# Optimization experiments

Hardware: AMD Instinct MI355X
Metric: run time of the kernel (lower is better)

The kernel has to match this reference:

```python
import jax, jax.numpy as jnp
import numpy as np

H, DH, C, K = 8, 128, 200, 15  # heads, head_dim, context_size, conv kernel
SCALE = DH ** -0.5
EPS = 1e-5


def layernorm(x, g, b):
    mu = jnp.mean(x, axis=-1, keepdims=True)
    var = jnp.mean(jnp.square(x - mu), axis=-1, keepdims=True)
    return (x - mu) * jax.lax.rsqrt(var + EPS) * g + b


def feedforward(x, ln_g, ln_b, up_w, up_b, down_w, down_b):
    h = layernorm(x, ln_g, ln_b)
    h = jax.nn.silu(h @ up_w + up_b)
    return h @ down_w + down_b


def attention(x, dist, ln_g, ln_b, wq, wkv, wo, wo_b, rel_emb):
    h = layernorm(x, ln_g, ln_b)
    b, f, d = h.shape
    nb = f // C  # num_features chosen divisible by context_size (no remainder path)
    q = (h @ wq).reshape(b, nb, C, H, DH).transpose(0, 1, 3, 2, 4)   # [b,nb,H,C,dh]
    kv = h @ wkv
    k, v = jnp.split(kv, 2, axis=-1)
    k = k.reshape(b, nb, C, H, DH).transpose(0, 1, 3, 2, 4)
    v = v.reshape(b, nb, C, H, DH).transpose(0, 1, 3, 2, 4)
    rel = rel_emb[dist]                                              # [C,C,dh]
    pos_attn = jnp.einsum('bnhid,ijd->bnhij', q, rel) * SCALE
    scores = jnp.einsum('bnhid,bnhjd->bnhij', q, k) * SCALE + pos_attn
    probs = jax.nn.softmax(scores, axis=-1)
    out = jnp.einsum('bnhij,bnhjd->bnhid', probs, v)
    out = out.transpose(0, 1, 3, 2, 4).reshape(b, f, H * DH)
    return out @ wo + wo_b


def conv_module(x, ln_g, ln_b, up_w, up_b, dw_w, bn_g, bn_b, bn_mean, bn_var, down_w, down_b):
    h = layernorm(x, ln_g, ln_b)
    h = h @ up_w + up_b                         # pointwise conv == linear; [b,L,2*inner]
    a, gate = jnp.split(h, 2, axis=-1)
    h = a * jax.nn.sigmoid(gate)                # GLU over channel dim
    h = h.transpose(0, 2, 1)                    # [b,inner,L]
    pad = K // 2
    h = jax.lax.conv_general_dilated(
        h, dw_w[:, None, :], window_strides=(1,), padding=[(pad, pad)],
        dimension_numbers=('NCH', 'OIH', 'NCH'), feature_group_count=h.shape[1])
    # BatchNorm1d in eval mode (running stats)
    h = (h - bn_mean[None, :, None]) * jax.lax.rsqrt(bn_var[None, :, None] + EPS)
    h = h * bn_g[None, :, None] + bn_b[None, :, None]
    h = jax.nn.silu(h)
    h = h.transpose(0, 2, 1) @ down_w + down_b  # [b,L,hidden]
    return h


def block_forward(x, attention_dists,
                  ff1_ln_g, ff1_ln_b, ff1_up_w, ff1_up_b, ff1_down_w, ff1_down_b,
                  attn_ln_g, attn_ln_b, wq, wkv, wo, wo_b, rel_emb,
                  conv_ln_g, conv_ln_b, conv_up_w, conv_up_b, dw_w,
                  bn_g, bn_b, bn_mean, bn_var, conv_down_w, conv_down_b,
                  ff2_ln_g, ff2_ln_b, ff2_up_w, ff2_up_b, ff2_down_w, ff2_down_b,
                  post_ln_g, post_ln_b):
    x = 0.5 * feedforward(x, ff1_ln_g, ff1_ln_b, ff1_up_w, ff1_up_b, ff1_down_w, ff1_down_b) + x
    x = attention(x, attention_dists, attn_ln_g, attn_ln_b, wq, wkv, wo, wo_b, rel_emb) + x
    x = conv_module(x, conv_ln_g, conv_ln_b, conv_up_w, conv_up_b, dw_w,
                    bn_g, bn_b, bn_mean, bn_var, conv_down_w, conv_down_b) + x
    x = 0.5 * feedforward(x, ff2_ln_g, ff2_ln_b, ff2_up_w, ff2_up_b, ff2_down_w, ff2_down_b) + x
    return layernorm(x, post_ln_g, post_ln_b)


def setup_inputs() -> dict:
    key = jax.random.key(0)
    ks = iter(jax.random.split(key, 40))
    d, dff, inner = 1024, 4096, 2048
    r = lambda shape, s=0.02: (jax.random.normal(next(ks), shape, jnp.float32) * s)
    inp = {
        'x': jax.random.normal(next(ks), (8, 2000, d), jnp.float32),
        'attention_dists': jax.random.randint(next(ks), (C, C), 0, 1025, jnp.int32),
        'ff1_ln_g': jnp.ones((d,)), 'ff1_ln_b': jnp.zeros((d,)),
        'ff1_up_w': r((d, dff)), 'ff1_up_b': jnp.zeros((dff,)),
        'ff1_down_w': r((dff, d)), 'ff1_down_b': jnp.zeros((d,)),
        'attn_ln_g': jnp.ones((d,)), 'attn_ln_b': jnp.zeros((d,)),
        'wq': r((d, H * DH)), 'wkv': r((d, 2 * H * DH)),
        'wo': r((H * DH, d)), 'wo_b': jnp.zeros((d,)),
        'rel_emb': r((2 * 512 + 1, DH)),
        'conv_ln_g': jnp.ones((d,)), 'conv_ln_b': jnp.zeros((d,)),
        'conv_up_w': r((d, 2 * inner)), 'conv_up_b': jnp.zeros((2 * inner,)),
        'dw_w': r((inner, K)),
        'bn_g': jnp.ones((inner,)), 'bn_b': jnp.zeros((inner,)),
        'bn_mean': r((inner,)), 'bn_var': jax.random.uniform(next(ks), (inner,), jnp.float32) + 0.5,
        'conv_down_w': r((inner, d)), 'conv_down_b': jnp.zeros((d,)),
        'ff2_ln_g': jnp.ones((d,)), 'ff2_ln_b': jnp.zeros((d,)),
        'ff2_up_w': r((d, dff)), 'ff2_up_b': jnp.zeros((dff,)),
        'ff2_down_w': r((dff, d)), 'ff2_down_b': jnp.zeros((d,)),
        'post_ln_g': jnp.ones((d,)), 'post_ln_b': jnp.zeros((d,)),
    }
    return inp


def reference(x, attention_dists,
              ff1_ln_g, ff1_ln_b, ff1_up_w, ff1_up_b, ff1_down_w, ff1_down_b,
              attn_ln_g, attn_ln_b, wq, wkv, wo, wo_b, rel_emb,
              conv_ln_g, conv_ln_b, conv_up_w, conv_up_b, dw_w,
              bn_g, bn_b, bn_mean, bn_var, conv_down_w, conv_down_b,
              ff2_ln_g, ff2_ln_b, ff2_up_w, ff2_up_b, ff2_down_w, ff2_down_b,
              post_ln_g, post_ln_b):
    return block_forward(x, attention_dists,
                         ff1_ln_g, ff1_ln_b, ff1_up_w, ff1_up_b, ff1_down_w, ff1_down_b,
                         attn_ln_g, attn_ln_b, wq, wkv, wo, wo_b, rel_emb,
                         conv_ln_g, conv_ln_b, conv_up_w, conv_up_b, dw_w,
                         bn_g, bn_b, bn_mean, bn_var, conv_down_w, conv_down_b,
                         ff2_ln_g, ff2_ln_b, ff2_up_w, ff2_up_b, ff2_down_w, ff2_down_b,
                         post_ln_g, post_ln_b)
```

## Files before the change

kernel.cpp:

```cpp
#include <hip/hip_runtime.h>

typedef unsigned short u16;
typedef unsigned int u32;
using short8 = __attribute__((ext_vector_type(8))) short;
using floatx4 = __attribute__((ext_vector_type(4))) float;

#define DMODEL 1024
#define DFF 4096
#define INNER 2048
#define DH 128
#define CTX 200
#define R_TOT 16000
#define ABN 40
#define AROWS (ABN * CTX)
#define AM (ABN * 8)
#define SCALE_Q 0.08838834764831845f

__device__ __forceinline__ u16 f2bf(float f) {
    union { float f; u32 u; } v; v.f = f;
    u32 r = v.u + 0x7FFFu + ((v.u >> 16) & 1u);
    return (u16)(r >> 16);
}
__device__ __forceinline__ float bf2f(u16 u) {
    union { u32 u; float f; } v; v.u = ((u32)u) << 16; return v.f;
}
__device__ __forceinline__ float sigmoidf_(float x) { return 1.f / (1.f + __expf(-x)); }

__device__ __forceinline__ void load_lds16(const void* g, void* l) {
    __builtin_amdgcn_global_load_lds((const __attribute__((address_space(1))) u32*)g,
                                     (__attribute__((address_space(3))) u32*)l, 16, 0, 0);
}

__device__ __forceinline__ void xcd_stripe_remap(int& bx, int& by) {
    const int gx = gridDim.x;
    const int gxs = gx >> 3;
    const int id = blockIdx.y * gx + blockIdx.x;
    const int xcd = id & 7;
    const int local = id >> 3;
    bx = xcd * gxs + (local % gxs);
    by = local / gxs;
}

template <int MODE>
__global__ __launch_bounds__(256, 4) void k_g(const u16* __restrict__ A, int lda,
                                              const u16* __restrict__ Bt, int ldb,
                                              const float* __restrict__ bias, float alpha,
                                              void* out, int ldc, const float* resid, int M,
                                              int N, int K) {
    __shared__ __align__(128) char lds[32768];
    int bx, by;
    xcd_stripe_remap(bx, by);
    const int row0 = bx * 128, col0 = by * 128;
    if (row0 >= M) return;
    const int lane = threadIdx.x & 63;
    const int wave = threadIdx.x >> 6;
    const int wrow = (wave >> 1) * 64;
    const int wcol = (wave & 1) * 64;
    const int lr = lane & 15;
    const int kg = lane >> 4;
    const int nt = K >> 6;

    const char* sA[4];
    const char* sB[4];
#pragma unroll
    for (int r = 0; r < 4; ++r) {
        int o = r * 4096 + wave * 1024 + lane * 16;
        int row = o >> 7;
        int srcb = (o & 127) ^ ((row & 7) << 4);
        int ga = row0 + row;
        ga = (ga < M) ? ga : M - 1;
        sA[r] = (const char*)A + (size_t)ga * ((size_t)lda * 2) + srcb;
        int gb = col0 + row;
        gb = (gb < N) ? gb : N - 1;
        sB[r] = (const char*)Bt + (size_t)gb * ((size_t)ldb * 2) + srcb;
    }
    floatx4 acc[4][4];
#pragma unroll
    for (int i = 0; i < 4; ++i)
#pragma unroll
        for (int j = 0; j < 4; ++j) acc[i][j] = (floatx4){0.f, 0.f, 0.f, 0.f};

    for (int t = 0; t < nt; ++t) {
        const int kb = t << 7;
#pragma unroll
        for (int r = 0; r < 4; ++r) {
            load_lds16(sA[r] + kb, lds + r * 4096 + wave * 1024);
            load_lds16(sB[r] + kb, lds + 16384 + r * 4096 + wave * 1024);
        }
        asm volatile("s_waitcnt vmcnt(0)" ::: "memory");
        __builtin_amdgcn_s_barrier();
#pragma unroll
        for (int ks = 0; ks < 2; ++ks) {
            short8 av[4], bv[4];
#pragma unroll
            for (int mi = 0; mi < 4; ++mi) {
                int row = wrow + mi * 16 + lr;
                int cb = (ks * 64 + kg * 16) ^ ((row & 7) << 4);
                av[mi] = *(const short8*)(lds + row * 128 + cb);
            }
#pragma unroll
            for (int ni = 0; ni < 4; ++ni) {
                int row = wcol + ni * 16 + lr;
                int cb = (ks * 64 + kg * 16) ^ ((row & 7) << 4);
                bv[ni] = *(const short8*)(lds + 16384 + row * 128 + cb);
            }
#pragma unroll
            for (int mi = 0; mi < 4; ++mi)
#pragma unroll
                for (int ni = 0; ni < 4; ++ni)
                    acc[mi][ni] = __builtin_amdgcn_mfma_f32_16x16x32_bf16(av[mi], bv[ni],
                                                                          acc[mi][ni], 0, 0, 0);
        }
        asm volatile("s_waitcnt lgkmcnt(0)" ::: "memory");
        __builtin_amdgcn_s_barrier();
    }
    u16* ob = (u16*)out;
    float* of = (float*)out;
#pragma unroll
    for (int mi = 0; mi < 4; ++mi)
#pragma unroll
        for (int ni = 0; ni < 4; ++ni)
#pragma unroll
            for (int rr = 0; rr < 4; ++rr) {
                const int r = row0 + wrow + mi * 16 + kg * 4 + rr;
                const int c = col0 + wcol + ni * 16 + lr;
                const float v = acc[mi][ni][rr];
                if (MODE == 3) {
                    float t = v + ((c & 1) ? bias[2048 + (c >> 1)] : bias[c >> 1]);
                    float g = __shfl_xor(t, 1);
                    if (!(c & 1) && r < M)
                        ob[(size_t)r * ldc + (c >> 1)] = f2bf(t * sigmoidf_(g));
                } else {
                    if (r >= M) continue;
                    size_t idx = (size_t)r * ldc + c;
                    float bb = bias ? bias[c] : 0.f;
                    if (MODE == 0) {
                        ob[idx] = f2bf(alpha * v + bb);
                    } else if (MODE == 1) {
                        float t = v + bb;
                        ob[idx] = f2bf(t * sigmoidf_(t));
                    } else {
                        of[idx] = alpha * (v + bb) + resid[idx];
                    }
                }
            }
}

template <typename RowMap>
__device__ __forceinline__ void stage_tile_s(const char* __restrict__ src, RowMap rowoff,
                                             int nrows, int row0, int k0b, char* tile) {
    const int lane = threadIdx.x & 63;
    const int wave = threadIdx.x >> 6;
#pragma unroll
    for (int r = 0; r < 4; ++r) {
        int o = r * 4096 + wave * 1024 + lane * 16;
        int row = o >> 7;
        int srcb = (o & 127) ^ ((row & 7) << 4);
        int grow = row0 + row;
        grow = (grow < nrows) ? grow : (nrows - 1);
        load_lds16(src + rowoff(grow) + k0b + srcb, tile + r * 4096 + wave * 1024);
    }
}

template <typename RMA, typename RMB, typename Epi>
__device__ __forceinline__ void gemm_core_s(const char* __restrict__ A, RMA rma, int a_rows,
                                            const char* __restrict__ B, RMB rmb, int b_rows,
                                            int K, int row0, int col0, char* lds, Epi epi) {
    const int lane = threadIdx.x & 63;
    const int wave = threadIdx.x >> 6;
    const int wrow = (wave >> 1) * 64;
    const int wcol = (wave & 1) * 64;
    const int lr = lane & 15;
    const int kg = lane >> 4;
    const int nt = K >> 6;

    floatx4 acc[4][4];
#pragma unroll
    for (int i = 0; i < 4; ++i)
#pragma unroll
        for (int j = 0; j < 4; ++j) acc[i][j] = (floatx4){0.f, 0.f, 0.f, 0.f};

    for (int t = 0; t < nt; ++t) {
        const int kb = t << 7;
        stage_tile_s(A, rma, a_rows, row0, kb, lds);
        stage_tile_s(B, rmb, b_rows, col0, kb, lds + 16384);
        asm volatile("s_waitcnt vmcnt(0)" ::: "memory");
        __builtin_amdgcn_s_barrier();
#pragma unroll
        for (int ks = 0; ks < 2; ++ks) {
            short8 av[4], bv[4];
#pragma unroll
            for (int mi = 0; mi < 4; ++mi) {
                int row = wrow + mi * 16 + lr;
                int cb = (ks * 64 + kg * 16) ^ ((row & 7) << 4);
                av[mi] = *(const short8*)(lds + row * 128 + cb);
            }
#pragma unroll
            for (int ni = 0; ni < 4; ++ni) {
                int row = wcol + ni * 16 + lr;
                int cb = (ks * 64 + kg * 16) ^ ((row & 7) << 4);
                bv[ni] = *(const short8*)(lds + 16384 + row * 128 + cb);
            }
#pragma unroll
            for (int mi = 0; mi < 4; ++mi)
#pragma unroll
                for (int ni = 0; ni < 4; ++ni)
                    acc[mi][ni] = __builtin_amdgcn_mfma_f32_16x16x32_bf16(av[mi], bv[ni],
                                                                          acc[mi][ni], 0, 0, 0);
        }
        asm volatile("s_waitcnt lgkmcnt(0)" ::: "memory");
        __builtin_amdgcn_s_barrier();
    }
#pragma unroll
    for (int mi = 0; mi < 4; ++mi)
#pragma unroll
        for (int ni = 0; ni < 4; ++ni)
#pragma unroll
            for (int rr = 0; rr < 4; ++rr)
                epi(row0 + wrow + mi * 16 + kg * 4 + rr, col0 + wcol + ni * 16 + lr,
                    acc[mi][ni][rr]);
}

__global__ __launch_bounds__(256, 4) void k_qk(const u16* __restrict__ q,
                                               const u16* __restrict__ kvc,
                                               u16* __restrict__ sc, int bn0) {
    __shared__ __align__(128) char lds[32768];
    const int z = blockIdx.z, bnl = z >> 3, h = z & 7;
    const char* A = (const char*)(q + ((size_t)(bn0 + bnl) * CTX) * DMODEL + h * DH);
    const char* B = (const char*)(kvc + ((size_t)bnl * CTX) * (2 * DMODEL) + h * DH);
    u16* out = sc + (size_t)z * CTX * 256;
    gemm_core_s(A, [](int r) { return (size_t)r * (DMODEL * 2); }, CTX, B,
                [](int r) { return (size_t)r * (4 * DMODEL); }, CTX, DH, blockIdx.x * 128,
                blockIdx.y * 128, lds, [&](int r, int c, float v) {
                    if (r < CTX) out[(size_t)r * 256 + c] = f2bf(v);
                });
}

__global__ __launch_bounds__(256, 4) void k_pos(const u16* __restrict__ q,
                                                const u16* __restrict__ rel,
                                                u16* __restrict__ sc, int m0) {
    __shared__ __align__(128) char lds[32768];
    const int i = blockIdx.z;
    const char* B = (const char*)(rel + (size_t)i * CTX * DH);
    u16* out = sc + i * 256;
    gemm_core_s((const char*)q,
                [=](int r) {
                    int m = m0 + r;
                    return (size_t)(((m >> 3) * CTX + i) * DMODEL + (m & 7) * DH) * 2;
                },
                AM, B, [](int r) { return (size_t)r * (DH * 2); }, CTX, DH, blockIdx.x * 128,
                blockIdx.y * 128, lds, [&](int r, int c, float v) {
                    if (r < AM) {
                        size_t idx = (size_t)r * (CTX * 256) + c;
                        out[idx] = f2bf(bf2f(out[idx]) + v);
                    }
                });
}

__global__ __launch_bounds__(256, 4) void k_pv(const u16* __restrict__ P,
                                               const u16* __restrict__ vT,
                                               u16* __restrict__ attn, int bn0) {
    __shared__ __align__(128) char lds[32768];
    const int z = blockIdx.z;
    u16* out = attn + ((size_t)(bn0 + (z >> 3)) * CTX) * DMODEL + (z & 7) * DH;
    const char* A = (const char*)(P + (size_t)z * CTX * 256);
    const char* B = (const char*)(vT + (size_t)z * DH * 256);
    gemm_core_s(A, [](int r) { return (size_t)r * 512; }, CTX, B,
                [](int r) { return (size_t)r * 512; }, DH, 256, blockIdx.x * 128, 0, lds,
                [&](int r, int c, float v) {
                    if (r < CTX) out[(size_t)r * DMODEL + c] = f2bf(v);
                });
}

template <bool OUTF32>
__global__ __launch_bounds__(256) void k_ln(const float* __restrict__ x,
                                            const float* __restrict__ g,
                                            const float* __restrict__ b, void* __restrict__ out) {
    const int row = blockIdx.x, t = threadIdx.x, lane = t & 63, wv = t >> 6;
    const float4 v = ((const float4*)(x + (size_t)row * DMODEL))[t];
    float s = v.x + v.y + v.z + v.w;
    float q = v.x * v.x + v.y * v.y + v.z * v.z + v.w * v.w;
#pragma unroll
    for (int off = 32; off > 0; off >>= 1) { s += __shfl_down(s, off); q += __shfl_down(q, off); }
    __shared__ float rs_[4], rq_[4];
    if (lane == 0) { rs_[wv] = s; rq_[wv] = q; }
    __syncthreads();
    s = rs_[0] + rs_[1] + rs_[2] + rs_[3];
    q = rq_[0] + rq_[1] + rq_[2] + rq_[3];
    const float mu = s * (1.f / DMODEL);
    const float rstd = rsqrtf(q * (1.f / DMODEL) - mu * mu + 1e-5f);
    const float4 gv = ((const float4*)g)[t];
    const float4 bv = ((const float4*)b)[t];
    float o0 = (v.x - mu) * rstd * gv.x + bv.x;
    float o1 = (v.y - mu) * rstd * gv.y + bv.y;
    float o2 = (v.z - mu) * rstd * gv.z + bv.z;
    float o3 = (v.w - mu) * rstd * gv.w + bv.w;
    if (OUTF32) {
        ((float4*)out)[(size_t)row * 256 + t] = make_float4(o0, o1, o2, o3);
    } else {
        ushort4 r4;
        r4.x = f2bf(o0); r4.y = f2bf(o1); r4.z = f2bf(o2); r4.w = f2bf(o3);
        ((ushort4*)out)[(size_t)row * 256 + t] = r4;
    }
}

__global__ __launch_bounds__(256) void k_softmax(u16* __restrict__ sc) {
    const size_t row = blockIdx.x;
    const int t = threadIdx.x, lane = t & 63, wv = t >> 6;
    float v = (t < CTX) ? bf2f(sc[row * 256 + t]) : -3.0e38f;
    float m = v;
#pragma unroll
    for (int off = 32; off > 0; off >>= 1) m = fmaxf(m, __shfl_down(m, off));
    __shared__ float rm[4], rsum[4];
    if (lane == 0) rm[wv] = m;
    __syncthreads();
    m = fmaxf(fmaxf(rm[0], rm[1]), fmaxf(rm[2], rm[3]));
    float e = (t < CTX) ? __expf(v - m) : 0.f;
    float s = e;
#pragma unroll
    for (int off = 32; off > 0; off >>= 1) s += __shfl_down(s, off);
    if (lane == 0) rsum[wv] = s;
    __syncthreads();
    s = rsum[0] + rsum[1] + rsum[2] + rsum[3];
    sc[row * 256 + t] = f2bf(e / s);
}

__global__ __launch_bounds__(256) void k_dwconv(const u16* __restrict__ in,
                                                const float* __restrict__ w,
                                                const float* __restrict__ bng,
                                                const float* __restrict__ bnb,
                                                const float* __restrict__ bnm,
                                                const float* __restrict__ bnv,
                                                u16* __restrict__ out) {
    const int b = blockIdx.z, lt = blockIdx.x, cg = blockIdx.y;
    const int c = cg * 256 + threadIdx.x;
    const int l0 = lt * 16;
    __shared__ u16 s[30][256];
#pragma unroll
    for (int rr = 0; rr < 30; ++rr) {
        int l = l0 + rr - 7;
        u16 v = 0;
        if (l >= 0 && l < 2000) v = in[((size_t)b * 2000 + l) * 2048 + c];
        s[rr][threadIdx.x] = v;
    }
    __syncthreads();
    float wv[15];
#pragma unroll
    for (int k = 0; k < 15; ++k) wv[k] = w[c * 15 + k];
    const float sc = rsqrtf(bnv[c] + 1e-5f) * bng[c];
    const float mean = bnm[c], bb = bnb[c];
#pragma unroll
    for (int l = 0; l < 16; ++l) {
        float acc = 0.f;
#pragma unroll
        for (int k = 0; k < 15; ++k) acc += bf2f(s[l + k][threadIdx.x]) * wv[k];
        float h = (acc - mean) * sc + bb;
        h = h * sigmoidf_(h);
        out[((size_t)b * 2000 + l0 + l) * 2048 + c] = f2bf(h);
    }
}

template <bool PAIR>
__global__ __launch_bounds__(256) void k_wt(const float* __restrict__ w, u16* __restrict__ wt,
                                            int K, int N) {
    __shared__ float tile[32][33];
    const int k0 = blockIdx.x * 32, n0 = blockIdx.y * 32;
    const int tx = threadIdx.x & 31, ty = threadIdx.x >> 5;
#pragma unroll
    for (int i = 0; i < 32; i += 8) tile[ty + i][tx] = w[(size_t)(k0 + ty + i) * N + n0 + tx];
    __syncthreads();
#pragma unroll
    for (int i = 0; i < 32; i += 8) {
        int n = n0 + ty + i;
        int pn = PAIR ? ((n < 2048) ? 2 * n : 2 * (n - 2048) + 1) : n;
        wt[(size_t)pn * K + k0 + tx] = f2bf(tile[tx][ty + i]);
    }
}

__global__ void k_rel(const float* __restrict__ emb, const int* __restrict__ dist,
                      u16* __restrict__ rel) {
    const int bid = blockIdx.x;
    const int d = dist[bid];
    rel[(size_t)bid * DH + threadIdx.x] = f2bf(emb[(size_t)d * DH + threadIdx.x]);
}

__global__ __launch_bounds__(256) void k_vt(const u16* __restrict__ kvc, u16* __restrict__ vT) {
    __shared__ u16 t_[64 * 130];
    const int z = blockIdx.x, jt = blockIdx.y;
    const int bnl = z >> 3, h = z & 7;
    const int j0 = jt * 64;
    for (int idx = threadIdx.x; idx < 8192; idx += 256) {
        int j = idx >> 7, dh = idx & 127;
        int jj = j0 + j;
        u16 val = 0;
        if (jj < CTX) val = kvc[((size_t)(bnl * CTX + jj)) * (2 * DMODEL) + DMODEL + h * DH + dh];
        t_[j * 130 + dh] = val;
    }
    __syncthreads();
    for (int idx = threadIdx.x; idx < 8192; idx += 256) {
        int dh = idx >> 6, j = idx & 63;
        vT[((size_t)z * DH + dh) * 256 + j0 + j] = t_[j * 130 + dh];
    }
}

__global__ void k_fill(float* o, int n, float v) {
    int i = blockIdx.x * 256 + threadIdx.x;
    if (i < n) o[i] = v;
}

extern "C" void kernel_launch(void* const* d_in, const int* in_sizes, int n_in, void* d_out,
                              int out_size, void* d_ws, size_t ws_size, hipStream_t stream) {
    const float* x_in = (const float*)d_in[0];
    const int* dists = (const int*)d_in[1];
    const float* ff1_ln_g = (const float*)d_in[2];
    const float* ff1_ln_b = (const float*)d_in[3];
    const float* ff1_up_w = (const float*)d_in[4];
    const float* ff1_up_b = (const float*)d_in[5];
    const float* ff1_down_w = (const float*)d_in[6];
    const float* ff1_down_b = (const float*)d_in[7];
    const float* attn_ln_g = (const float*)d_in[8];
    const float* attn_ln_b = (const float*)d_in[9];
    const float* wq = (const float*)d_in[10];
    const float* wkv = (const float*)d_in[11];
    const float* wo = (const float*)d_in[12];
    const float* wo_b = (const float*)d_in[13];
    const float* rel_emb = (const float*)d_in[14];
    const float* conv_ln_g = (const float*)d_in[15];
    const float* conv_ln_b = (const float*)d_in[16];
    const float* conv_up_w = (const float*)d_in[17];
    const float* conv_up_b = (const float*)d_in[18];
    const float* dw_w = (const float*)d_in[19];
    const float* bn_g = (const float*)d_in[20];
    const float* bn_b = (const float*)d_in[21];
    const float* bn_mean = (const float*)d_in[22];
    const float* bn_var = (const float*)d_in[23];
    const float* conv_down_w = (const float*)d_in[24];
    const float* conv_down_b = (const float*)d_in[25];
    const float* ff2_ln_g = (const float*)d_in[26];
    const float* ff2_ln_b = (const float*)d_in[27];
    const float* ff2_up_w = (const float*)d_in[28];
    const float* ff2_up_b = (const float*)d_in[29];
    const float* ff2_down_w = (const float*)d_in[30];
    const float* ff2_down_b = (const float*)d_in[31];
    const float* post_ln_g = (const float*)d_in[32];
    const float* post_ln_b = (const float*)d_in[33];

    char* W = (char*)d_ws;
    size_t off = 0;
    auto alloc = [&](size_t bytes) {
        char* p = W + off;
        off += (bytes + 255) & ~(size_t)255;
        return (u16*)p;
    };
    u16* slot = alloc((size_t)4096 * 1024 * 2);
    u16* ln_buf = alloc((size_t)R_TOT * DMODEL * 2);
    u16* arena = alloc((size_t)R_TOT * DFF * 2);
    u16* mid = arena;
    u16* rel_bf = arena;
    u16* bufA = rel_bf + (size_t)CTX * CTX * DH;
    u16* bufB = bufA + (size_t)AROWS * 2 * DMODEL;
    u16* smid = bufB + (size_t)R_TOT * DMODEL;
    u16* vT = smid + (size_t)AM * CTX * 256;
    u16* gluo = arena;
    u16* convo = arena + (size_t)R_TOT * INNER;
    float* xs = (float*)d_out;

    if (ws_size < off) {
        k_fill<<<(out_size + 255) / 256, 256, 0, stream>>>((float*)d_out, out_size, 31337.f);
        return;
    }

    auto WT = [&](const float* s, int K, int N) {
        k_wt<false><<<dim3(K / 32, N / 32), 256, 0, stream>>>(s, slot, K, N);
    };

    const dim3 gUP(128, 32);
    const dim3 gSQ(128, 8);
    const dim3 gKV(64, 16);

    auto ff_block = [&](const float* lng, const float* lnb, const float* upw, const float* upb,
                        const float* dnw, const float* dnb, const float* resid,
                        const float* xsrc) {
        k_ln<false><<<R_TOT, 256, 0, stream>>>(xsrc, lng, lnb, ln_buf);
        WT(upw, 1024, 4096);
        k_g<1><<<gUP, 256, 0, stream>>>(ln_buf, DMODEL, slot, DMODEL, upb, 1.f, mid, DFF,
                                        nullptr, R_TOT, DFF, DMODEL);
        WT(dnw, 4096, 1024);
        k_g<2><<<gSQ, 256, 0, stream>>>(mid, DFF, slot, DFF, dnb, 0.5f, xs, DMODEL, resid,
                                        R_TOT, DMODEL, DFF);
    };

    ff_block(ff1_ln_g, ff1_ln_b, ff1_up_w, ff1_up_b, ff1_down_w, ff1_down_b, x_in, x_in);

    k_ln<false><<<R_TOT, 256, 0, stream>>>(xs, attn_ln_g, attn_ln_b, ln_buf);
    k_rel<<<CTX * CTX, 128, 0, stream>>>(rel_emb, dists, rel_bf);
    WT(wq, 1024, 1024);
    k_g<0><<<gSQ, 256, 0, stream>>>(ln_buf, DMODEL, slot, DMODEL, nullptr, SCALE_Q, bufB,
                                    DMODEL, nullptr, R_TOT, DMODEL, DMODEL);
    WT(wkv, 1024, 2048);
    for (int h = 0; h < 2; ++h) {
        const int bn0 = h * ABN, m0 = bn0 * 8;
        const u16* lnc = ln_buf + (size_t)bn0 * CTX * DMODEL;
        k_g<0><<<gKV, 256, 0, stream>>>(lnc, DMODEL, slot, DMODEL, nullptr, 1.f, bufA,
                                        2 * DMODEL, nullptr, AROWS, 2 * DMODEL, DMODEL);
        k_vt<<<dim3(AM, 4), 256, 0, stream>>>(bufA, vT);
        k_qk<<<dim3(2, 2, AM), 256, 0, stream>>>(bufB, bufA, smid, bn0);
        k_pos<<<dim3(3, 2, CTX), 256, 0, stream>>>(bufB, rel_bf, smid, m0);
        k_softmax<<<AM * CTX, 256, 0, stream>>>(smid);
        k_pv<<<dim3(2, 1, AM), 256, 0, stream>>>(smid, vT, bufB, bn0);
    }
    WT(wo, 1024, 1024);
    k_g<2><<<gSQ, 256, 0, stream>>>(bufB, DMODEL, slot, DMODEL, wo_b, 1.f, xs, DMODEL, xs,
                                    R_TOT, DMODEL, DMODEL);

    k_ln<false><<<R_TOT, 256, 0, stream>>>(xs, conv_ln_g, conv_ln_b, ln_buf);
    k_wt<true><<<dim3(1024 / 32, 4096 / 32), 256, 0, stream>>>(conv_up_w, slot, 1024, 4096);
    k_g<3><<<gUP, 256, 0, stream>>>(ln_buf, DMODEL, slot, DMODEL, conv_up_b, 1.f, gluo, INNER,
                                    nullptr, R_TOT, DFF, DMODEL);
    k_dwconv<<<dim3(125, 8, 8), 256, 0, stream>>>(gluo, dw_w, bn_g, bn_b, bn_mean, bn_var,
                                                  convo);
    WT(conv_down_w, 2048, 1024);
    k_g<2><<<gSQ, 256, 0, stream>>>(convo, INNER, slot, INNER, conv_down_b, 1.f, xs, DMODEL, xs,
                                    R_TOT, DMODEL, INNER);

    ff_block(ff2_ln_g, ff2_ln_b, ff2_up_w, ff2_up_b, ff2_down_w, ff2_down_b, xs, xs);

    k_ln<true><<<R_TOT, 256, 0, stream>>>(xs, post_ln_g, post_ln_b, d_out);
}
```

Before: 1.698 ms.

## Replace 128x128 GEMM with 256x256 8-wave double-buffered pipelined kernel

Swaps the 128x128 tile GEMM (256 threads, single LDS buffer, full wait each k-step) for a 256x256 tile kernel with 8 waves, 128KB of LDS in two stages, and interleaved prefetch of the next k-tile while MFMAs run, raising MFMA priority with s_setprio. The LDS layout becomes 64-byte rows with a new XOR swizzle. Larger tiles cut global/LDS traffic per FLOP and the pipelining hides load latency. In exchange occupancy drops to one block per CU, and edge handling for M=8000/16000 stays as clamped rows, with fewer blocks for small GEMMs.

```diff
diff --git a/kernel.cpp b/kernel.cpp
--- a/kernel.cpp
+++ b/kernel.cpp
@@ -42,82 +42,159 @@
 }
 
 template <int MODE>
-__global__ __launch_bounds__(256, 4) void k_g(const u16* __restrict__ A, int lda,
-                                              const u16* __restrict__ Bt, int ldb,
-                                              const float* __restrict__ bias, float alpha,
-                                              void* out, int ldc, const float* resid, int M,
-                                              int N, int K) {
-    __shared__ __align__(128) char lds[32768];
+__global__ __launch_bounds__(512, 1) void k_g8(const u16* __restrict__ A, int lda,
+                                               const u16* __restrict__ Bt, int ldb,
+                                               const float* __restrict__ bias, float alpha,
+                                               void* out, int ldc, const float* resid, int M,
+                                               int N, int K) {
+    __shared__ __align__(128) char lds[131072];
     int bx, by;
     xcd_stripe_remap(bx, by);
-    const int row0 = bx * 128, col0 = by * 128;
+    const int row0 = bx * 256, col0 = by * 256;
     if (row0 >= M) return;
-    const int lane = threadIdx.x & 63;
-    const int wave = threadIdx.x >> 6;
-    const int wrow = (wave >> 1) * 64;
-    const int wcol = (wave & 1) * 64;
+    const int tid = threadIdx.x;
+    const int lane = tid & 63;
+    const int wave = tid >> 6;
+    const int wrow = (wave >> 2) * 128;
+    const int wcol = (wave & 3) * 64;
     const int lr = lane & 15;
     const int kg = lane >> 4;
     const int nt = K >> 6;
 
-    const char* sA[4];
-    const char* sB[4];
-#pragma unroll
-    for (int r = 0; r < 4; ++r) {
-        int o = r * 4096 + wave * 1024 + lane * 16;
-        int row = o >> 7;
-        int srcb = (o & 127) ^ ((row & 7) << 4);
+    const char* pA[2];
+    const char* pB[2];
+    int so[2];
+#pragma unroll
+    for (int r = 0; r < 2; ++r) {
+        int o = r * 8192 + tid * 16;
+        int row = o >> 6;
+        int col = (o & 63) ^ (((row >> 1) & 3) << 4);
         int ga = row0 + row;
         ga = (ga < M) ? ga : M - 1;
-        sA[r] = (const char*)A + (size_t)ga * ((size_t)lda * 2) + srcb;
         int gb = col0 + row;
         gb = (gb < N) ? gb : N - 1;
-        sB[r] = (const char*)Bt + (size_t)gb * ((size_t)ldb * 2) + srcb;
-    }
-    floatx4 acc[4][4];
-#pragma unroll
-    for (int i = 0; i < 4; ++i)
+        pA[r] = (const char*)A + (size_t)ga * ((size_t)lda * 2) + col;
+        pB[r] = (const char*)Bt + (size_t)gb * ((size_t)ldb * 2) + col;
+        so[r] = o;
+    }
+    int aoff[8], boff[4];
+#pragma unroll
+    for (int mi = 0; mi < 8; ++mi) {
+        int row = wrow + mi * 16 + lr;
+        aoff[mi] = row * 64 + ((kg * 16) ^ (((row >> 1) & 3) << 4));
+    }
+#pragma unroll
+    for (int ni = 0; ni < 4; ++ni) {
+        int row = wcol + ni * 16 + lr;
+        boff[ni] = row * 64 + ((kg * 16) ^ (((row >> 1) & 3) << 4));
+    }
+    floatx4 acc[8][4];
+#pragma unroll
+    for (int i = 0; i < 8; ++i)
 #pragma unroll
         for (int j = 0; j < 4; ++j) acc[i][j] = (floatx4){0.f, 0.f, 0.f, 0.f};
 
+#define STAGE_A(buf, kbyte, half)                                               \
+    {                                                                           \
+        load_lds16(pA[0] + (kbyte) + (half)*64, (buf) + (half)*16384 + so[0]);  \
+        load_lds16(pA[1] + (kbyte) + (half)*64, (buf) + (half)*16384 + so[1]);  \
+    }
+#define STAGE_B(buf, kbyte, half)                                                       \
+    {                                                                                   \
+        load_lds16(pB[0] + (kbyte) + (half)*64, (buf) + 32768 + (half)*16384 + so[0]);  \
+        load_lds16(pB[1] + (kbyte) + (half)*64, (buf) + 32768 + (half)*16384 + so[1]);  \
+    }
+
+    STAGE_A(lds, 0, 0);
+    STAGE_B(lds, 0, 0);
+    STAGE_A(lds, 0, 1);
+    STAGE_B(lds, 0, 1);
+
     for (int t = 0; t < nt; ++t) {
-        const int kb = t << 7;
-#pragma unroll
-        for (int r = 0; r < 4; ++r) {
-            load_lds16(sA[r] + kb, lds + r * 4096 + wave * 1024);
-            load_lds16(sB[r] + kb, lds + 16384 + r * 4096 + wave * 1024);
+        char* cur = lds + (t & 1) * 65536;
+        char* nxt = lds + ((t + 1) & 1) * 65536;
+        const int kb = (t + 1) << 7;
+        const bool pf = (t + 1 < nt);
+        short8 av[4], bv[4];
+        if (pf) {
+            STAGE_A(nxt, kb, 0);
+            asm volatile("s_waitcnt vmcnt(6)" ::: "memory");
+        } else {
+            asm volatile("s_waitcnt vmcnt(4)" ::: "memory");
         }
-        asm volatile("s_waitcnt vmcnt(0)" ::: "memory");
-        __builtin_amdgcn_s_barrier();
-#pragma unroll
-        for (int ks = 0; ks < 2; ++ks) {
-            short8 av[4], bv[4];
-#pragma unroll
-            for (int mi = 0; mi < 4; ++mi) {
-                int row = wrow + mi * 16 + lr;
-                int cb = (ks * 64 + kg * 16) ^ ((row & 7) << 4);
-                av[mi] = *(const short8*)(lds + row * 128 + cb);
-            }
-#pragma unroll
-            for (int ni = 0; ni < 4; ++ni) {
-                int row = wcol + ni * 16 + lr;
-                int cb = (ks * 64 + kg * 16) ^ ((row & 7) << 4);
-                bv[ni] = *(const short8*)(lds + 16384 + row * 128 + cb);
-            }
-#pragma unroll
-            for (int mi = 0; mi < 4; ++mi)
-#pragma unroll
-                for (int ni = 0; ni < 4; ++ni)
-                    acc[mi][ni] = __builtin_amdgcn_mfma_f32_16x16x32_bf16(av[mi], bv[ni],
-                                                                          acc[mi][ni], 0, 0, 0);
+        __builtin_amdgcn_s_barrier();
+#pragma unroll
+        for (int ni = 0; ni < 4; ++ni) bv[ni] = *(const short8*)(cur + 32768 + boff[ni]);
+#pragma unroll
+        for (int mi = 0; mi < 4; ++mi) av[mi] = *(const short8*)(cur + aoff[mi]);
+        asm volatile("s_waitcnt lgkmcnt(0)" ::: "memory");
+        __builtin_amdgcn_sched_barrier(0);
+        __builtin_amdgcn_s_setprio(1);
+#pragma unroll
+        for (int mi = 0; mi < 4; ++mi)
+#pragma unroll
+            for (int ni = 0; ni < 4; ++ni)
+                acc[mi][ni] =
+                    __builtin_amdgcn_mfma_f32_16x16x32_bf16(av[mi], bv[ni], acc[mi][ni], 0, 0, 0);
+        __builtin_amdgcn_s_setprio(0);
+        __builtin_amdgcn_s_barrier();
+        if (pf) STAGE_B(nxt, kb, 0);
+#pragma unroll
+        for (int mi = 0; mi < 4; ++mi) av[mi] = *(const short8*)(cur + aoff[4 + mi]);
+        asm volatile("s_waitcnt lgkmcnt(0)" ::: "memory");
+        __builtin_amdgcn_sched_barrier(0);
+        __builtin_amdgcn_s_setprio(1);
+#pragma unroll
+        for (int mi = 0; mi < 4; ++mi)
+#pragma unroll
+            for (int ni = 0; ni < 4; ++ni)
+                acc[4 + mi][ni] =
+                    __builtin_amdgcn_mfma_f32_16x16x32_bf16(av[mi], bv[ni], acc[4 + mi][ni], 0, 0, 0);
+        __builtin_amdgcn_s_setprio(0);
+        __builtin_amdgcn_s_barrier();
+        if (pf) {
+            STAGE_A(nxt, kb, 1);
+            asm volatile("s_waitcnt vmcnt(6)" ::: "memory");
+        } else {
+            asm volatile("s_waitcnt vmcnt(0)" ::: "memory");
         }
+        __builtin_amdgcn_s_barrier();
+#pragma unroll
+        for (int ni = 0; ni < 4; ++ni) bv[ni] = *(const short8*)(cur + 49152 + boff[ni]);
+#pragma unroll
+        for (int mi = 0; mi < 4; ++mi) av[mi] = *(const short8*)(cur + 16384 + aoff[mi]);
         asm volatile("s_waitcnt lgkmcnt(0)" ::: "memory");
-        __builtin_amdgcn_s_barrier();
-    }
+        __builtin_amdgcn_sched_barrier(0);
+        __builtin_amdgcn_s_setprio(1);
+#pragma unroll
+        for (int mi = 0; mi < 4; ++mi)
+#pragma unroll
+            for (int ni = 0; ni < 4; ++ni)
+                acc[mi][ni] =
+                    __builtin_amdgcn_mfma_f32_16x16x32_bf16(av[mi], bv[ni], acc[mi][ni], 0, 0, 0);
+        __builtin_amdgcn_s_setprio(0);
+        __builtin_amdgcn_s_barrier();
+        if (pf) STAGE_B(nxt, kb, 1);
+#pragma unroll
+        for (int mi = 0; mi < 4; ++mi) av[mi] = *(const short8*)(cur + 16384 + aoff[4 + mi]);
+        asm volatile("s_waitcnt lgkmcnt(0)" ::: "memory");
+        __builtin_amdgcn_sched_barrier(0);
+        __builtin_amdgcn_s_setprio(1);
+#pragma unroll
+        for (int mi = 0; mi < 4; ++mi)
+#pragma unroll
+            for (int ni = 0; ni < 4; ++ni)
+                acc[4 + mi][ni] =
+                    __builtin_amdgcn_mfma_f32_16x16x32_bf16(av[mi], bv[ni], acc[4 + mi][ni], 0, 0, 0);
+        __builtin_amdgcn_s_setprio(0);
+        __builtin_amdgcn_s_barrier();
+    }
+#undef STAGE_A
+#undef STAGE_B
     u16* ob = (u16*)out;
     float* of = (float*)out;
 #pragma unroll
-    for (int mi = 0; mi < 4; ++mi)
+    for (int mi = 0; mi < 8; ++mi)
 #pragma unroll
         for (int ni = 0; ni < 4; ++ni)
 #pragma unroll
@@ -126,10 +203,10 @@
                 const int c = col0 + wcol + ni * 16 + lr;
                 const float v = acc[mi][ni][rr];
                 if (MODE == 3) {
-                    float t = v + ((c & 1) ? bias[2048 + (c >> 1)] : bias[c >> 1]);
-                    float g = __shfl_xor(t, 1);
+                    float tt = v + ((c & 1) ? bias[2048 + (c >> 1)] : bias[c >> 1]);
+                    float g = __shfl_xor(tt, 1);
                     if (!(c & 1) && r < M)
-                        ob[(size_t)r * ldc + (c >> 1)] = f2bf(t * sigmoidf_(g));
+                        ob[(size_t)r * ldc + (c >> 1)] = f2bf(tt * sigmoidf_(g));
                 } else {
                     if (r >= M) continue;
                     size_t idx = (size_t)r * ldc + c;
@@ -137,8 +214,8 @@
                     if (MODE == 0) {
                         ob[idx] = f2bf(alpha * v + bb);
                     } else if (MODE == 1) {
-                        float t = v + bb;
-                        ob[idx] = f2bf(t * sigmoidf_(t));
+                        float tt = v + bb;
+                        ob[idx] = f2bf(tt * sigmoidf_(tt));
                     } else {
                         of[idx] = alpha * (v + bb) + resid[idx];
                     }
@@ -474,20 +551,20 @@
         k_wt<false><<<dim3(K / 32, N / 32), 256, 0, stream>>>(s, slot, K, N);
     };
 
-    const dim3 gUP(128, 32);
-    const dim3 gSQ(128, 8);
-    const dim3 gKV(64, 16);
+    const dim3 gUP(64, 16);
+    const dim3 gSQ(64, 4);
+    const dim3 gKV(32, 8);
 
     auto ff_block = [&](const float* lng, const float* lnb, const float* upw, const float* upb,
                         const float* dnw, const float* dnb, const float* resid,
                         const float* xsrc) {
         k_ln<false><<<R_TOT, 256, 0, stream>>>(xsrc, lng, lnb, ln_buf);
         WT(upw, 1024, 4096);
-        k_g<1><<<gUP, 256, 0, stream>>>(ln_buf, DMODEL, slot, DMODEL, upb, 1.f, mid, DFF,
-                                        nullptr, R_TOT, DFF, DMODEL);
+        k_g8<1><<<gUP, 512, 0, stream>>>(ln_buf, DMODEL, slot, DMODEL, upb, 1.f, mid, DFF,
+                                         nullptr, R_TOT, DFF, DMODEL);
         WT(dnw, 4096, 1024);
-        k_g<2><<<gSQ, 256, 0, stream>>>(mid, DFF, slot, DFF, dnb, 0.5f, xs, DMODEL, resid,
-                                        R_TOT, DMODEL, DFF);
+        k_g8<2><<<gSQ, 512, 0, stream>>>(mid, DFF, slot, DFF, dnb, 0.5f, xs, DMODEL, resid,
+                                         R_TOT, DMODEL, DFF);
     };
 
     ff_block(ff1_ln_g, ff1_ln_b, ff1_up_w, ff1_up_b, ff1_down_w, ff1_down_b, x_in, x_in);
@@ -495,14 +572,14 @@
     k_ln<false><<<R_TOT, 256, 0, stream>>>(xs, attn_ln_g, attn_ln_b, ln_buf);
     k_rel<<<CTX * CTX, 128, 0, stream>>>(rel_emb, dists, rel_bf);
     WT(wq, 1024, 1024);
-    k_g<0><<<gSQ, 256, 0, stream>>>(ln_buf, DMODEL, slot, DMODEL, nullptr, SCALE_Q, bufB,
-                                    DMODEL, nullptr, R_TOT, DMODEL, DMODEL);
+    k_g8<0><<<gSQ, 512, 0, stream>>>(ln_buf, DMODEL, slot, DMODEL, nullptr, SCALE_Q, bufB,
+                                     DMODEL, nullptr, R_TOT, DMODEL, DMODEL);
     WT(wkv, 1024, 2048);
     for (int h = 0; h < 2; ++h) {
         const int bn0 = h * ABN, m0 = bn0 * 8;
         const u16* lnc = ln_buf + (size_t)bn0 * CTX * DMODEL;
-        k_g<0><<<gKV, 256, 0, stream>>>(lnc, DMODEL, slot, DMODEL, nullptr, 1.f, bufA,
-                                        2 * DMODEL, nullptr, AROWS, 2 * DMODEL, DMODEL);
+        k_g8<0><<<gKV, 512, 0, stream>>>(lnc, DMODEL, slot, DMODEL, nullptr, 1.f, bufA,
+                                         2 * DMODEL, nullptr, AROWS, 2 * DMODEL, DMODEL);
         k_vt<<<dim3(AM, 4), 256, 0, stream>>>(bufA, vT);
         k_qk<<<dim3(2, 2, AM), 256, 0, stream>>>(bufB, bufA, smid, bn0);
         k_pos<<<dim3(3, 2, CTX), 256, 0, stream>>>(bufB, rel_bf, smid, m0);
@@ -510,18 +587,18 @@
         k_pv<<<dim3(2, 1, AM), 256, 0, stream>>>(smid, vT, bufB, bn0);
     }
     WT(wo, 1024, 1024);
-    k_g<2><<<gSQ, 256, 0, stream>>>(bufB, DMODEL, slot, DMODEL, wo_b, 1.f, xs, DMODEL, xs,
-                                    R_TOT, DMODEL, DMODEL);
+    k_g8<2><<<gSQ, 512, 0, stream>>>(bufB, DMODEL, slot, DMODEL, wo_b, 1.f, xs, DMODEL, xs,
+                                     R_TOT, DMODEL, DMODEL);
 
     k_ln<false><<<R_TOT, 256, 0, stream>>>(xs, conv_ln_g, conv_ln_b, ln_buf);
     k_wt<true><<<dim3(1024 / 32, 4096 / 32), 256, 0, stream>>>(conv_up_w, slot, 1024, 4096);
-    k_g<3><<<gUP, 256, 0, stream>>>(ln_buf, DMODEL, slot, DMODEL, conv_up_b, 1.f, gluo, INNER,
-                                    nullptr, R_TOT, DFF, DMODEL);
+    k_g8<3><<<gUP, 512, 0, stream>>>(ln_buf, DMODEL, slot, DMODEL, conv_up_b, 1.f, gluo, INNER,
+                                     nullptr, R_TOT, DFF, DMODEL);
     k_dwconv<<<dim3(125, 8, 8), 256, 0, stream>>>(gluo, dw_w, bn_g, bn_b, bn_mean, bn_var,
                                                   convo);
     WT(conv_down_w, 2048, 1024);
-    k_g<2><<<gSQ, 256, 0, stream>>>(convo, INNER, slot, INNER, conv_down_b, 1.f, xs, DMODEL, xs,
-                                    R_TOT, DMODEL, INNER);
+    k_g8<2><<<gSQ, 512, 0, stream>>>(convo, INNER, slot, INNER, conv_down_b, 1.f, xs, DMODEL,
+                                     xs, R_TOT, DMODEL, INNER);
 
     ff_block(ff2_ln_g, ff2_ln_b, ff2_up_w, ff2_up_b, ff2_down_w, ff2_down_b, xs, xs);
 
```

Measured after the change: 1.933 ms. +13.8%, slower.
